# Kernel optimization log

Hardware: AMD Instinct MI355X
Metric: run time of the kernel (lower is better)

The kernel has to match this reference:

```python
import jax, jax.numpy as jnp
import numpy as np

D = 1024; DI = 2048; HS = 16; PS = DI // HS; NS = 64; KC = 4; CHUNK = 64
HA = 16; HKV = 4; PA = D // HA; MLP_MULT = 4; ROPE_BASE = 10000.0
B_SZ = 2; L_SEQ = 2048


def rms_norm(x):
    eps = jnp.asarray(jnp.finfo(x.dtype).eps, x.dtype)
    return x * jax.lax.rsqrt(jnp.mean(jnp.square(x), axis=-1, keepdims=True) + eps)


def silu(x):
    return x * jax.nn.sigmoid(x)


def apply_rope(x, cos, sin):
    half = x.shape[-1] // 2
    x1, x2 = x[..., :half], x[..., half:]
    return jnp.concatenate([x1 * cos + x2 * sin, -x1 * sin + x2 * cos], axis=-1)


def selective_scan(x, A, Bm, Cm, dt, chunk):
    # x: [B,L,H,P], Bm/Cm: [B,L,H,N], A/dt: [H]. L must be a multiple of chunk.
    Bb, L, H, P = x.shape
    N = Bm.shape[-1]
    decay = jnp.exp(A * dt)  # [H]
    nc = L // chunk
    xp = x.reshape(Bb, nc, chunk, H, P).transpose(0, 1, 3, 2, 4)   # [B,nc,H,cs,P]
    Bp = Bm.reshape(Bb, nc, chunk, H, N).transpose(0, 1, 3, 2, 4)  # [B,nc,H,cs,N]
    Cp = Cm.reshape(Bb, nc, chunk, H, N).transpose(0, 1, 3, 2, 4)
    x_dt = xp * dt[None, None, :, None, None]
    idx = jnp.arange(chunk)
    diff = idx[:, None] - idx[None, :]
    # intra-chunk causal decay matrix L_mat: [H,cs,cs]
    Lm = jnp.where(diff >= 0, decay[:, None, None] ** jnp.maximum(diff, 0), 0.0)
    CB = jnp.einsum('bchqn,bchkn->bchqk', Cp, Bp)
    y_diag = jnp.einsum('bchqk,bchkp->bchqp', CB * Lm[None, None], x_dt)
    # per-chunk states
    decay_rev = decay[:, None] ** (chunk - 1 - idx)[None, :]  # [H,cs]
    states = jnp.einsum('bchtn,bchtp->bchnp', Bp * decay_rev[None, None, :, :, None], x_dt)
    # inter-chunk propagation
    ci = jnp.arange(nc)
    shift = ci[:, None] - ci[None, :] - 1
    cdec = decay ** chunk
    M = jnp.where(shift >= 0, cdec[:, None, None] ** jnp.maximum(shift, 0), 0.0)  # [H,nc,nc]
    h_carry = jnp.einsum('hij,bjhnp->bihnp', M, states)
    decay_out = decay[:, None] ** (idx + 1)[None, :]  # [H,cs]
    y_off = jnp.einsum('bchtn,bchnp->bchtp', Cp, h_carry) * decay_out[None, None, :, :, None]
    y = (y_diag + y_off).transpose(0, 1, 3, 2, 4).reshape(Bb, L, H, P)
    return y


def mlp(n, fc_w, proj_w):
    h = jax.nn.relu(n @ fc_w)
    return jnp.square(h) @ proj_w


def setup_inputs() -> dict:
    key = jax.random.key(0)
    ks = jax.random.split(key, 24)
    w = lambda k, shp, s=0.02: jax.random.normal(k, shp, jnp.float32) * s
    dt_init = jax.random.uniform(ks[0], (HS,), jnp.float32, 0.001, 0.1)
    dt_bias = dt_init + jnp.log(-jnp.expm1(-dt_init))  # inverse softplus
    return {
        'x': jax.random.normal(ks[1], (B_SZ, L_SEQ, D), jnp.float32),
        'in_proj_w': w(ks[2], (D, 2 * DI)),
        'conv_w': w(ks[3], (DI, KC), 0.2),
        'conv_b': jnp.zeros((DI,), jnp.float32),
        'B_proj_w': w(ks[4], (D, HS * NS)),
        'C_proj_w': w(ks[5], (D, HS * NS)),
        'dt_bias': dt_bias,
        'A_log': jnp.log(jnp.arange(1, HS + 1, dtype=jnp.float32)),
        'D_param': jnp.ones((HS,), jnp.float32),
        'out_proj_w': w(ks[6], (DI, D)),
        'resid_mix_m': jnp.stack([jnp.ones(D), jnp.zeros(D)]).astype(jnp.float32),
        'mamba_scale': jnp.ones((D,), jnp.float32),
        'm_fc_w': w(ks[7], (D, MLP_MULT * D)),
        'm_proj_w': w(ks[8], (MLP_MULT * D, D)),
        'm_mlp_scale': jnp.ones((D,), jnp.float32),
        'resid_mix_a': jnp.stack([jnp.ones(D), jnp.zeros(D)]).astype(jnp.float32),
        'q_w': w(ks[9], (D, D)),
        'k_w': w(ks[10], (D, HKV * PA)),
        'v_w': w(ks[11], (D, HKV * PA)),
        'o_w': w(ks[12], (D, D)),
        'q_gain': jnp.full((HA,), 1.0, jnp.float32),
        'attn_scale': jnp.ones((D,), jnp.float32),
        'a_fc_w': w(ks[13], (D, MLP_MULT * D)),
        'a_proj_w': w(ks[14], (MLP_MULT * D, D)),
        'a_mlp_scale': jnp.ones((D,), jnp.float32),
    }


def reference(x, in_proj_w, conv_w, conv_b, B_proj_w, C_proj_w, dt_bias, A_log, D_param, out_proj_w, resid_mix_m, mamba_scale, m_fc_w, m_proj_w, m_mlp_scale, resid_mix_a, q_w, k_w, v_w, o_w, q_gain, attn_scale, a_fc_w, a_proj_w, a_mlp_scale):
    Bb, L, _ = x.shape
    x0 = x
    # ---- Mamba block ----
    xm = resid_mix_m[0][None, None] * x + resid_mix_m[1][None, None] * x0
    n = rms_norm(xm)
    vg = n @ in_proj_w
    value, gate = vg[..., :DI], vg[..., DI:]
    v_t = value.transpose(0, 2, 1)  # [B, DI, L]
    v_conv = jax.lax.conv_general_dilated(
        v_t, conv_w[:, None, :], (1,), [(KC - 1, 0)],
        feature_group_count=DI, dimension_numbers=('NCH', 'OIH', 'NCH')) + conv_b[None, :, None]
    value = silu(v_conv).transpose(0, 2, 1).reshape(Bb, L, HS, PS)
    Bm = (xm @ B_proj_w).reshape(Bb, L, HS, NS)  # B/C use pre-norm (mixed) input
    Cm = (xm @ C_proj_w).reshape(Bb, L, HS, NS)
    dt = jax.nn.softplus(dt_bias)
    A = -jnp.exp(A_log)
    y = selective_scan(value, A, Bm, Cm, dt, CHUNK)
    y = y + D_param[None, None, :, None] * value
    y = (y.reshape(Bb, L, DI) * silu(gate)) @ out_proj_w
    xm = xm + mamba_scale[None, None] * y
    xm = xm + m_mlp_scale[None, None] * mlp(rms_norm(xm), m_fc_w, m_proj_w)
    # ---- Attention block ----
    xa = resid_mix_a[0][None, None] * xm + resid_mix_a[1][None, None] * x0
    n = rms_norm(xa)
    q = (n @ q_w).reshape(Bb, L, HA, PA).transpose(0, 2, 1, 3)
    k = (n @ k_w).reshape(Bb, L, HKV, PA).transpose(0, 2, 1, 3)
    v = (n @ v_w).reshape(Bb, L, HKV, PA).transpose(0, 2, 1, 3)
    q = rms_norm(q); k = rms_norm(k)
    inv_freq = 1.0 / (ROPE_BASE ** (jnp.arange(0, PA, 2, dtype=jnp.float32) / PA))
    f = jnp.outer(jnp.arange(L, dtype=jnp.float32), inv_freq)
    cos, sin = jnp.cos(f)[None, None], jnp.sin(f)[None, None]
    q = apply_rope(q, cos, sin) * q_gain[None, :, None, None]
    k = apply_rope(k, cos, sin)
    G = HA // HKV
    k = jnp.repeat(k, G, axis=1); v = jnp.repeat(v, G, axis=1)
    s = jnp.einsum('bhqd,bhkd->bhqk', q, k) / np.float32(np.sqrt(PA))
    mask = jnp.tril(jnp.ones((L, L), bool))
    s = jnp.where(mask[None, None], s, jnp.asarray(-jnp.inf, s.dtype))
    att = jax.nn.softmax(s, axis=-1)
    y = jnp.einsum('bhqk,bhkd->bhqd', att, v).transpose(0, 2, 1, 3).reshape(Bb, L, D)
    xa = xa + attn_scale[None, None] * (y @ o_w)
    xa = xa + a_mlp_scale[None, None] * mlp(rms_norm(xa), a_fc_w, a_proj_w)
    return xa
```

## Files before the change

### kernel.cpp

```cpp
#include <hip/hip_runtime.h>
#include <hip/hip_bf16.h>
#include <math.h>

#define D_ 1024
#define DI_ 2048
#define HS_ 16
#define PS_ 128
#define NS_ 64
#define HA_ 16
#define HKV_ 4
#define PA_ 64
#define B_ 2
#define L_ 2048
#define NT_ 4096
#define NC_ 32
#define RMS_EPS_ 1.1920929e-7f

typedef __attribute__((ext_vector_type(8))) short short8;
typedef __attribute__((ext_vector_type(4))) float f32x4;

#define GLOAD_LDS16(gp, lp)                                                        \
  __builtin_amdgcn_global_load_lds(                                               \
      (const __attribute__((address_space(1))) unsigned int*)(gp),                \
      (__attribute__((address_space(3))) unsigned int*)(lp), 16, 0, 0)

__global__ __launch_bounds__(256) void transpose_cvt(
    const float* __restrict__ W, __hip_bfloat16* __restrict__ Wt, int K, int N, int ldw) {
  __shared__ float t[32][33];
  int n0 = blockIdx.x * 32, k0 = blockIdx.y * 32;
  int tx = threadIdx.x & 31, ty = threadIdx.x >> 5;
#pragma unroll
  for (int i = 0; i < 4; i++)
    t[ty + i * 8][tx] = W[(size_t)(k0 + ty + i * 8) * ldw + n0 + tx];
  __syncthreads();
#pragma unroll
  for (int i = 0; i < 4; i++)
    Wt[(size_t)(n0 + ty + i * 8) * K + k0 + tx] = __float2bfloat16(t[tx][ty + i * 8]);
}

template<int MODE>
__global__ __launch_bounds__(512) void gemm256_k32(
    const unsigned short* __restrict__ A, const unsigned short* __restrict__ Wt,
    __hip_bfloat16* __restrict__ Cb, int N, int K) {
  __shared__ unsigned short As[3][256 * 32];
  __shared__ unsigned short Bs[3][256 * 32];
  int lid = blockIdx.x;
  int x = lid & 7, r = lid >> 3;
  int bm = ((x >> 2) * 8 + (r & 7)) * 256;
  int bn = ((x & 3) * 4 + (r >> 3)) * 256;
  int tid = threadIdx.x;
  int w = tid >> 6, l = tid & 63;
  int wr = w >> 2, wc = w & 3;
  int l15 = l & 15, lg = l >> 4;
  int rr = tid >> 2, ss = tid & 3;

  f32x4 acc[8][4];
#pragma unroll
  for (int i = 0; i < 8; i++)
#pragma unroll
    for (int j = 0; j < 4; j++) acc[i][j] = (f32x4){0.f, 0.f, 0.f, 0.f};

  auto STAGE = [&](int kt, int nb) {
    int k0 = kt * 32;
#pragma unroll
    for (int p = 0; p < 2; p++) {
      int row = p * 128 + rr;
      int kq = ss ^ ((row >> 1) & 3);
      GLOAD_LDS16(A + (size_t)(bm + row) * K + k0 + kq * 8, &As[nb][row * 32 + ss * 8]);
    }
#pragma unroll
    for (int p = 0; p < 2; p++) {
      int row = p * 128 + rr;
      int kq = ss ^ ((row >> 1) & 3);
      GLOAD_LDS16(Wt + (size_t)(bn + row) * K + k0 + kq * 8, &Bs[nb][row * 32 + ss * 8]);
    }
  };

  int KT = K >> 5;
  STAGE(0, 0);
  STAGE(1, 1);
  int buf = 0;
  for (int t = 0; t < KT; ++t) {
    asm volatile("s_waitcnt vmcnt(4)" ::: "memory");
    __builtin_amdgcn_s_barrier();
    __builtin_amdgcn_sched_barrier(0);
    if (t + 2 < KT) STAGE(t + 2, (t + 2) % 3);
    short8 bf[4];
#pragma unroll
    for (int j = 0; j < 4; j++) {
      int row = wc * 64 + j * 16 + l15;
      bf[j] = *(const short8*)&Bs[buf][row * 32 + ((lg ^ ((row >> 1) & 3)) << 3)];
    }
#pragma unroll
    for (int i = 0; i < 8; i++) {
      int row = wr * 128 + i * 16 + l15;
      short8 af = *(const short8*)&As[buf][row * 32 + ((lg ^ ((row >> 1) & 3)) << 3)];
#pragma unroll
      for (int j = 0; j < 4; j++)
        acc[i][j] = __builtin_amdgcn_mfma_f32_16x16x32_bf16(af, bf[j], acc[i][j], 0, 0, 0);
    }
    buf = (buf + 1) % 3;
  }
#pragma unroll
  for (int i = 0; i < 8; i++)
#pragma unroll
    for (int j = 0; j < 4; j++) {
      int gr = bm + wr * 128 + i * 16 + lg * 4;
      int gc = bn + wc * 64 + j * 16 + l15;
#pragma unroll
      for (int reg = 0; reg < 4; reg++) {
        float v = acc[i][j][reg];
        if (MODE == 1) { v = fmaxf(v, 0.f); v = v * v; }
        Cb[(size_t)(gr + reg) * N + gc] = __float2bfloat16(v);
      }
    }
}

template<int BN>
__global__ __launch_bounds__(256) void gemm_bf16_t(
    const unsigned short* __restrict__ A, const unsigned short* __restrict__ Wt,
    float* __restrict__ Cf, __hip_bfloat16* __restrict__ Cb,
    const float* __restrict__ baseb, const float* __restrict__ scale,
    int N, int K, int gn, int mode) {
  constexpr int nWc = BN / 64;
  constexpr int nWr = 4 / nWc;
  constexpr int MF  = 8 / nWr;
  __shared__ unsigned short As[2][128 * 64];
  __shared__ unsigned short Bs[2][BN * 64];
  int lid = blockIdx.x;
  int x = lid & 7, r = lid >> 3;
  int RN = gn >> 2;
  int bm = ((x >> 2) * 16 + (r & 15)) * 128;
  int bn = ((x & 3) * RN + (r >> 4)) * BN;
  int tid = threadIdx.x;
  int w = tid >> 6, l = tid & 63;
  int wr = w / nWc, wc = w % nWc;
  int l15 = l & 15, lg = l >> 4;
  f32x4 acc[MF][4];
#pragma unroll
  for (int i = 0; i < MF; i++)
#pragma unroll
    for (int j = 0; j < 4; j++) acc[i][j] = (f32x4){0.f, 0.f, 0.f, 0.f};
  int r_ = tid >> 3;
  int s_ = tid & 7;

  auto STAGE = [&](int k0, int nb) {
#pragma unroll
    for (int i = 0; i < 4; i++) {
      int rr = i * 32 + r_;
      int kq = s_ ^ (rr & 7);
      GLOAD_LDS16(A + (size_t)(bm + rr) * K + k0 + kq * 8, &As[nb][rr * 64 + s_ * 8]);
    }
#pragma unroll
    for (int i = 0; i < BN / 32; i++) {
      int rr = i * 32 + r_;
      int kq = s_ ^ (rr & 7);
      GLOAD_LDS16(Wt + (size_t)(bn + rr) * K + k0 + kq * 8, &Bs[nb][rr * 64 + s_ * 8]);
    }
  };

  STAGE(0, 0);
  __syncthreads();
  int cur = 0;
  for (int k0 = 0; k0 < K; k0 += 64) {
    if (k0 + 64 < K) STAGE(k0 + 64, cur ^ 1);
#pragma unroll
    for (int h = 0; h < 2; h++) {
      short8 af[MF], bfr[4];
#pragma unroll
      for (int i = 0; i < MF; i++) {
        int row = wr * (16 * MF) + i * 16 + l15;
        int c = h * 4 + lg;
        af[i] = *(const short8*)&As[cur][row * 64 + ((c ^ (row & 7)) << 3)];
      }
#pragma unroll
      for (int j = 0; j < 4; j++) {
        int row = wc * 64 + j * 16 + l15;
        int c = h * 4 + lg;
        bfr[j] = *(const short8*)&Bs[cur][row * 64 + ((c ^ (row & 7)) << 3)];
      }
#pragma unroll
      for (int i = 0; i < MF; i++)
#pragma unroll
        for (int j = 0; j < 4; j++)
          acc[i][j] = __builtin_amdgcn_mfma_f32_16x16x32_bf16(af[i], bfr[j], acc[i][j], 0, 0, 0);
    }
    __syncthreads();
    cur ^= 1;
  }
  int rb = lg * 4, cb2 = l15;
#pragma unroll
  for (int i = 0; i < MF; i++)
#pragma unroll
    for (int j = 0; j < 4; j++) {
      int gr = bm + wr * (16 * MF) + i * 16 + rb;
      int gc = bn + wc * 64 + j * 16 + cb2;
#pragma unroll
      for (int reg = 0; reg < 4; reg++) {
        float v = acc[i][j][reg];
        size_t idx = (size_t)(gr + reg) * N + gc;
        if (mode == 0) {
          Cf[idx] = v;
        } else if (mode == 1) {
          v = fmaxf(v, 0.f);
          Cb[idx] = __float2bfloat16(v * v);
        } else if (mode == 2) {
          Cb[idx] = __float2bfloat16(v);
        } else {
          Cf[idx] = baseb[idx] + scale[gc] * v;
        }
      }
    }
}

__global__ __launch_bounds__(256) void mix_rms_kernel(
    const float* __restrict__ a, const float* __restrict__ b2,
    const float* __restrict__ mix, float* __restrict__ xout,
    __hip_bfloat16* __restrict__ nbf, __hip_bfloat16* __restrict__ rawbf) {
  int row = blockIdx.x;
  size_t base = (size_t)row * D_;
  float v[4]; float ss = 0.f;
#pragma unroll
  for (int i = 0; i < 4; i++) {
    int d = threadIdx.x + i * 256;
    float val = mix[d] * a[base + d] + mix[D_ + d] * b2[base + d];
    v[i] = val; ss += val * val;
  }
  for (int o = 32; o > 0; o >>= 1) ss += __shfl_down(ss, o, 64);
  __shared__ float red[4];
  if ((threadIdx.x & 63) == 0) red[threadIdx.x >> 6] = ss;
  __syncthreads();
  float inv = rsqrtf((red[0] + red[1] + red[2] + red[3]) * (1.f / D_) + RMS_EPS_);
#pragma unroll
  for (int i = 0; i < 4; i++) {
    int d = threadIdx.x + i * 256;
    xout[base + d] = v[i];
    nbf[base + d] = __float2bfloat16(v[i] * inv);
    if (rawbf) rawbf[base + d] = __float2bfloat16(v[i]);
  }
}

__global__ __launch_bounds__(256) void rms_kernel(
    const float* __restrict__ a, __hip_bfloat16* __restrict__ nbf) {
  int row = blockIdx.x;
  size_t base = (size_t)row * D_;
  float v[4]; float ss = 0.f;
#pragma unroll
  for (int i = 0; i < 4; i++) {
    int d = threadIdx.x + i * 256;
    float val = a[base + d];
    v[i] = val; ss += val * val;
  }
  for (int o = 32; o > 0; o >>= 1) ss += __shfl_down(ss, o, 64);
  __shared__ float red[4];
  if ((threadIdx.x & 63) == 0) red[threadIdx.x >> 6] = ss;
  __syncthreads();
  float inv = rsqrtf((red[0] + red[1] + red[2] + red[3]) * (1.f / D_) + RMS_EPS_);
#pragma unroll
  for (int i = 0; i < 4; i++) {
    int d = threadIdx.x + i * 256;
    nbf[base + d] = __float2bfloat16(v[i] * inv);
  }
}

__global__ __launch_bounds__(256) void conv_silu_kernel(
    const __hip_bfloat16* __restrict__ vg, const float* __restrict__ cw,
    const float* __restrict__ cb, float* __restrict__ xv) {
  int idx = blockIdx.x * 256 + threadIdx.x;
  int c = idx & (DI_ - 1);
  int bl = idx >> 11;
  int l = bl & (L_ - 1);
  float acc = cb[c];
  float w0 = cw[c * 4 + 0], w1 = cw[c * 4 + 1], w2 = cw[c * 4 + 2], w3 = cw[c * 4 + 3];
  size_t rb = (size_t)bl * 4096 + c;
  if (l >= 3) acc += __bfloat162float(vg[rb - (size_t)3 * 4096]) * w0;
  if (l >= 2) acc += __bfloat162float(vg[rb - (size_t)2 * 4096]) * w1;
  if (l >= 1) acc += __bfloat162float(vg[rb - (size_t)1 * 4096]) * w2;
  acc += __bfloat162float(vg[rb]) * w3;
  xv[idx] = acc / (1.f + __expf(-acc));
}

__global__ __launch_bounds__(256) void scanA1_kernel(
    const float* __restrict__ xv, const __hip_bfloat16* __restrict__ BCm,
    const float* __restrict__ dt_bias, const float* __restrict__ A_log,
    float* __restrict__ st) {
  __shared__ __align__(16) float sm[4096 + 8192];
  float* Bs = sm;
  float* Xs = sm + 4096;
  int blk = blockIdx.x;
  int c = blk & 31, h = (blk >> 5) & 15, b = blk >> 9;
  float dt = log1pf(__expf(dt_bias[h]));
  float adt = -__expf(A_log[h]) * dt;
  int tid = threadIdx.x;
  int l0 = c * 64;
  size_t rB = ((size_t)(b * L_ + l0)) * 2048 + h * NS_;
#pragma unroll
  for (int i = 0; i < 16; i++) {
    int e = tid + i * 256;
    int t = e >> 6, n = e & 63;
    Bs[t * 64 + n] = __bfloat162float(BCm[rB + (size_t)t * 2048 + n]);
  }
  size_t rX = ((size_t)(b * L_ + l0)) * DI_ + h * PS_;
#pragma unroll
  for (int i = 0; i < 32; i++) {
    int e = tid + i * 256;
    int t = e >> 7, p = e & 127;
    Xs[t * 128 + p] = xv[rX + (size_t)t * DI_ + p];
  }
  __syncthreads();
  int pg = tid & 31;
  int ng = (tid >> 5) << 3;
  float acc[8][4];
#pragma unroll
  for (int nn = 0; nn < 8; nn++)
#pragma unroll
    for (int i = 0; i < 4; i++) acc[nn][i] = 0.f;
  for (int t = 0; t < 64; t++) {
    float dr = __expf(adt * (float)(63 - t));
    float4 x4 = *(const float4*)&Xs[t * 128 + pg * 4];
    float xd0 = x4.x * dr, xd1 = x4.y * dr, xd2 = x4.z * dr, xd3 = x4.w * dr;
#pragma unroll
    for (int nn = 0; nn < 8; nn++) {
      float bv = Bs[t * 64 + ng + nn];
      acc[nn][0] += bv * xd0; acc[nn][1] += bv * xd1;
      acc[nn][2] += bv * xd2; acc[nn][3] += bv * xd3;
    }
  }
  size_t sb = ((size_t)((b * HS_ + h) * NC_ + c)) * (NS_ * PS_);
#pragma unroll
  for (int nn = 0; nn < 8; nn++) {
    *(float4*)&st[sb + (size_t)(ng + nn) * PS_ + pg * 4] =
        make_float4(acc[nn][0] * dt, acc[nn][1] * dt, acc[nn][2] * dt, acc[nn][3] * dt);
  }
}

__global__ __launch_bounds__(256) void scanA2_kernel(
    const float* __restrict__ xv, const __hip_bfloat16* __restrict__ BCm,
    const float* __restrict__ dt_bias,
    const float* __restrict__ A_log, const float* __restrict__ D_param,
    float* __restrict__ y) {
  __shared__ __align__(16) float sm[4160 + 8192];
  float* Cb = sm;
  float* Bs = sm + 4160;
  float* Xs = sm + 4160;
  int blk = blockIdx.x;
  int c = blk & 31, h = (blk >> 5) & 15, b = blk >> 9;
  float dt = log1pf(__expf(dt_bias[h]));
  float adt = -__expf(A_log[h]) * dt;
  float Dp = D_param[h];
  int tid = threadIdx.x;
  int l0 = c * 64;
  size_t rB = ((size_t)(b * L_ + l0)) * 2048 + h * NS_;
#pragma unroll
  for (int i = 0; i < 16; i++) {
    int e = tid + i * 256;
    int t = e >> 6, n = e & 63;
    Bs[t * 64 + n] = __bfloat162float(BCm[rB + (size_t)t * 2048 + n]);
    Cb[t * 65 + n] = __bfloat162float(BCm[rB + 1024 + (size_t)t * 2048 + n]);
  }
  __syncthreads();
  int q = tid >> 2;
  int kb = (tid & 3) << 4;
  float cbl[16];
#pragma unroll
  for (int kk = 0; kk < 16; kk++) {
    int k = kb + kk;
    float a = 0.f;
    if (k <= q) {
      for (int n = 0; n < 64; n++) a += Cb[q * 65 + n] * Bs[k * 64 + n];
      a *= __expf(adt * (float)(q - k));
    }
    cbl[kk] = a;
  }
  __syncthreads();
#pragma unroll
  for (int kk = 0; kk < 16; kk++) Cb[q * 65 + kb + kk] = cbl[kk];
  size_t rX = ((size_t)(b * L_ + l0)) * DI_ + h * PS_;
#pragma unroll
  for (int i = 0; i < 32; i++) {
    int e = tid + i * 256;
    int t = e >> 7, p = e & 127;
    Xs[t * 128 + p] = xv[rX + (size_t)t * DI_ + p];
  }
  __syncthreads();
  int pg = tid & 31;
  int qg = (tid >> 5) << 3;
  float acc[8][4];
#pragma unroll
  for (int qq = 0; qq < 8; qq++)
#pragma unroll
    for (int i = 0; i < 4; i++) acc[qq][i] = 0.f;
  for (int k = 0; k < 64; k++) {
    float4 x4 = *(const float4*)&Xs[k * 128 + pg * 4];
#pragma unroll
    for (int qq = 0; qq < 8; qq++) {
      float s = Cb[(qg + qq) * 65 + k];
      acc[qq][0] += s * x4.x; acc[qq][1] += s * x4.y;
      acc[qq][2] += s * x4.z; acc[qq][3] += s * x4.w;
    }
  }
#pragma unroll
  for (int qq = 0; qq < 8; qq++) {
    int qr = qg + qq;
    float4 xq = *(const float4*)&Xs[qr * 128 + pg * 4];
    size_t yo = ((size_t)(b * L_ + l0 + qr)) * DI_ + h * PS_ + pg * 4;
    *(float4*)&y[yo] = make_float4(acc[qq][0] * dt + Dp * xq.x,
                                   acc[qq][1] * dt + Dp * xq.y,
                                   acc[qq][2] * dt + Dp * xq.z,
                                   acc[qq][3] * dt + Dp * xq.w);
  }
}

__global__ __launch_bounds__(256) void scanB1_kernel(
    float* __restrict__ st, const float* __restrict__ dt_bias,
    const float* __restrict__ A_log) {
  int slice = blockIdx.x & 3;
  int h = (blockIdx.x >> 2) & 15, b = blockIdx.x >> 6;
  float dt = log1pf(__expf(dt_bias[h]));
  float adt = -__expf(A_log[h]) * dt;
  float cdec = __expf(adt * 64.f);
  size_t base = ((size_t)(b * HS_ + h)) * NC_ * (NS_ * PS_) + slice * 2048 + threadIdx.x;
  float hreg[8];
#pragma unroll
  for (int j = 0; j < 8; j++) hreg[j] = 0.f;
  for (int c = 0; c < NC_; c++) {
    size_t o = base + (size_t)c * (NS_ * PS_);
#pragma unroll
    for (int j = 0; j < 8; j++) {
      float tmp = st[o + (size_t)j * 256];
      st[o + (size_t)j * 256] = hreg[j];
      hreg[j] = cdec * hreg[j] + tmp;
    }
  }
}

__global__ __launch_bounds__(256) void scanB2_kernel(
    const __hip_bfloat16* __restrict__ BCm, const float* __restrict__ st,
    const __hip_bfloat16* __restrict__ vg, const float* __restrict__ dt_bias,
    const float* __restrict__ A_log, const float* __restrict__ y,
    __hip_bfloat16* __restrict__ yout) {
  __shared__ float Cs[64 * 64];
  __shared__ __align__(16) float Hs[64 * 128];
  int blk = blockIdx.x;
  int c = blk & 31, h = (blk >> 5) & 15, b = blk >> 9;
  float dt = log1pf(__expf(dt_bias[h]));
  float adt = -__expf(A_log[h]) * dt;
  int tid = threadIdx.x;
  int l0 = c * 64;
  size_t rC = ((size_t)(b * L_ + l0)) * 2048 + 1024 + h * NS_;
#pragma unroll
  for (int i = 0; i < 16; i++) {
    int e = tid + i * 256;
    int t = e >> 6, n = e & 63;
    Cs[t * 64 + n] = __bfloat162float(BCm[rC + (size_t)t * 2048 + n]);
  }
  size_t sb = ((size_t)((b * HS_ + h) * NC_ + c)) * (NS_ * PS_);
#pragma unroll
  for (int i = 0; i < 32; i++) {
    int e = tid + i * 256;
    Hs[e] = st[sb + e];
  }
  __syncthreads();
  int pg = tid & 31;
  int tg = (tid >> 5) << 3;
  float acc[8][4];
#pragma unroll
  for (int tt = 0; tt < 8; tt++)
#pragma unroll
    for (int i = 0; i < 4; i++) acc[tt][i] = 0.f;
  for (int n = 0; n < 64; n++) {
    float4 h4 = *(const float4*)&Hs[n * 128 + pg * 4];
#pragma unroll
    for (int tt = 0; tt < 8; tt++) {
      float cv = Cs[(tg + tt) * 64 + n];
      acc[tt][0] += cv * h4.x; acc[tt][1] += cv * h4.y;
      acc[tt][2] += cv * h4.z; acc[tt][3] += cv * h4.w;
    }
  }
#pragma unroll
  for (int tt = 0; tt < 8; tt++) {
    int t = tg + tt;
    float dout = __expf(adt * (float)(t + 1));
    size_t row = (size_t)(b * L_ + l0 + t);
#pragma unroll
    for (int i = 0; i < 4; i++) {
      int p = pg * 4 + i;
      float g = __bfloat162float(vg[row * 4096 + 2048 + h * PS_ + p]);
      float yv = y[row * DI_ + h * PS_ + p] + acc[tt][i] * dout;
      yout[row * DI_ + h * PS_ + p] = __float2bfloat16(yv * (g / (1.f + __expf(-g))));
    }
  }
}

__global__ void rope_fill_kernel(float* __restrict__ cosb, float* __restrict__ sinb) {
  int idx = blockIdx.x * 256 + threadIdx.x;
  int i = idx & 31, l = idx >> 5;
  float inv = __expf(-(2.0f * (float)i / (float)PA_) * logf(10000.0f));
  float ang = (float)l * inv;
  cosb[idx] = cosf(ang);
  sinb[idx] = sinf(ang);
}

__global__ __launch_bounds__(256) void qknorm_rope_bf16_kernel(
    const float* __restrict__ src, int srcstride, int srcofs,
    __hip_bfloat16* __restrict__ dst, int nh,
    const float* __restrict__ cosb, const float* __restrict__ sinb,
    const float* __restrict__ gain) {
  int row = blockIdx.x * 4 + (threadIdx.x >> 6);
  int lane = threadIdx.x & 63;
  int h = row % nh;
  int tok = row / nh;
  int l = tok & (L_ - 1);
  float v = src[(size_t)tok * srcstride + srcofs + h * 64 + lane];
  float ss = v * v;
  for (int o = 32; o > 0; o >>= 1) ss += __shfl_xor(ss, o, 64);
  v *= rsqrtf(ss * (1.f / PA_) + RMS_EPS_);
  float partner = __shfl_xor(v, 32, 64);
  int i = lane & 31;
  float cth = cosb[l * 32 + i], sth = sinb[l * 32 + i];
  float out = (lane < 32) ? (v * cth + partner * sth) : (v * cth - partner * sth);
  if (gain) out *= gain[h];
  dst[(size_t)tok * (nh * 64) + h * 64 + lane] = __float2bfloat16(out);
}

__global__ __launch_bounds__(256) void attn_mfma_kernel(
    const unsigned short* __restrict__ qb, const unsigned short* __restrict__ kb,
    const unsigned short* __restrict__ vt, const float* __restrict__ qgain,
    __hip_bfloat16* __restrict__ ao) {
  __shared__ unsigned short Ks[64][72];
  __shared__ unsigned short Vs[64][72];
  __shared__ unsigned short Psm[4][16][72];
  int blk = blockIdx.x;
  int qi = blk & 15;
  int h  = (blk >> 4) & 15;
  int b  = blk >> 8;
  int hk = h >> 2;
  int tid = threadIdx.x;
  int w = tid >> 6, l = tid & 63;
  int l15 = l & 15, lg = l >> 4;
  int r0 = tid >> 3, s0 = tid & 7;
  float mstat = 8.0f * fabsf(qgain[h]);
  const unsigned short* kbase = kb + (size_t)b * L_ * (HKV_ * PA_) + hk * PA_ + s0 * 8;
  const unsigned short* vbase = vt + ((size_t)(b * HKV_ + hk) * PA_) * L_ + s0 * 8;

  for (int pass = 0; pass < 2; pass++) {
    int qt = pass ? (31 - qi) : qi;
    int q0 = qt * 64;
    int qw = q0 + w * 16;
    short8 qf[2];
    {
      size_t qrow = ((size_t)(b * L_ + qw + l15)) * (HA_ * PA_) + h * PA_;
      qf[0] = *(const short8*)&qb[qrow + lg * 8];
      qf[1] = *(const short8*)&qb[qrow + 32 + lg * 8];
    }
    f32x4 o_acc[4];
#pragma unroll
    for (int db = 0; db < 4; db++) o_acc[db] = (f32x4){0.f, 0.f, 0.f, 0.f};
    f32x4 lsum = (f32x4){0.f, 0.f, 0.f, 0.f};
    int nkt = qt + 1;
    short8 kr0 = *(const short8*)&kbase[(size_t)r0 * (HKV_ * PA_)];
    short8 kr1 = *(const short8*)&kbase[(size_t)(r0 + 32) * (HKV_ * PA_)];
    short8 vr0 = *(const short8*)&vbase[(size_t)r0 * L_];
    short8 vr1 = *(const short8*)&vbase[(size_t)(r0 + 32) * L_];
    for (int kt = 0; kt < nkt; kt++) {
      int k0 = kt * 64;
      __syncthreads();
      *(short8*)&Ks[r0][s0 * 8] = kr0;
      *(short8*)&Ks[r0 + 32][s0 * 8] = kr1;
      *(short8*)&Vs[r0][s0 * 8] = vr0;
      *(short8*)&Vs[r0 + 32][s0 * 8] = vr1;
      if (kt + 1 < nkt) {
        int k1 = k0 + 64;
        kr0 = *(const short8*)&kbase[(size_t)(k1 + r0) * (HKV_ * PA_)];
        kr1 = *(const short8*)&kbase[(size_t)(k1 + r0 + 32) * (HKV_ * PA_)];
        vr0 = *(const short8*)&vbase[(size_t)r0 * L_ + k1];
        vr1 = *(const short8*)&vbase[(size_t)(r0 + 32) * L_ + k1];
      }
      __syncthreads();
      f32x4 s_acc[4];
#pragma unroll
      for (int kb2 = 0; kb2 < 4; kb2++) {
        short8 b0 = *(const short8*)&Ks[kb2 * 16 + l15][lg * 8];
        short8 b1 = *(const short8*)&Ks[kb2 * 16 + l15][32 + lg * 8];
        f32x4 s = (f32x4){0.f, 0.f, 0.f, 0.f};
        s = __builtin_amdgcn_mfma_f32_16x16x32_bf16(qf[0], b0, s, 0, 0, 0);
        s = __builtin_amdgcn_mfma_f32_16x16x32_bf16(qf[1], b1, s, 0, 0, 0);
        s_acc[kb2] = s;
      }
      bool diag = (kt == qt);
#pragma unroll
      for (int kb2 = 0; kb2 < 4; kb2++) {
        int key = k0 + kb2 * 16 + l15;
#pragma unroll
        for (int reg = 0; reg < 4; reg++) {
          float p = __expf(s_acc[kb2][reg] * 0.125f - mstat);
          if (diag && key > qw + lg * 4 + reg) p = 0.f;
          lsum[reg] += p;
          __hip_bfloat16 hv = __float2bfloat16(p);
          Psm[w][lg * 4 + reg][kb2 * 16 + l15] = *(unsigned short*)&hv;
        }
      }
      asm volatile("s_waitcnt lgkmcnt(0)" ::: "memory");
#pragma unroll
      for (int ks = 0; ks < 2; ks++) {
        short8 pa = *(const short8*)&Psm[w][l15][ks * 32 + lg * 8];
#pragma unroll
        for (int db = 0; db < 4; db++) {
          short8 vb8 = *(const short8*)&Vs[db * 16 + l15][ks * 32 + lg * 8];
          o_acc[db] = __builtin_amdgcn_mfma_f32_16x16x32_bf16(pa, vb8, o_acc[db], 0, 0, 0);
        }
      }
    }
#pragma unroll
    for (int of = 1; of < 16; of <<= 1) {
      lsum[0] += __shfl_xor(lsum[0], of, 64);
      lsum[1] += __shfl_xor(lsum[1], of, 64);
      lsum[2] += __shfl_xor(lsum[2], of, 64);
      lsum[3] += __shfl_xor(lsum[3], of, 64);
    }
#pragma unroll
    for (int reg = 0; reg < 4; reg++) {
      float invl = 1.0f / lsum[reg];
      size_t row = (size_t)(b * L_ + qw + lg * 4 + reg);
#pragma unroll
      for (int db = 0; db < 4; db++)
        ao[row * D_ + h * PA_ + db * 16 + l15] = __float2bfloat16(o_acc[db][reg] * invl);
    }
  }
}

extern "C" void kernel_launch(void* const* d_in, const int* in_sizes, int n_in,
                              void* d_out, int out_size, void* d_ws, size_t ws_size,
                              hipStream_t stream) {
  (void)in_sizes; (void)n_in; (void)out_size; (void)ws_size;
  const float* x           = (const float*)d_in[0];
  const float* in_proj_w   = (const float*)d_in[1];
  const float* conv_w      = (const float*)d_in[2];
  const float* conv_b      = (const float*)d_in[3];
  const float* B_proj_w    = (const float*)d_in[4];
  const float* C_proj_w    = (const float*)d_in[5];
  const float* dt_bias     = (const float*)d_in[6];
  const float* A_log       = (const float*)d_in[7];
  const float* D_param     = (const float*)d_in[8];
  const float* out_proj_w  = (const float*)d_in[9];
  const float* resid_mix_m = (const float*)d_in[10];
  const float* mamba_scale = (const float*)d_in[11];
  const float* m_fc_w      = (const float*)d_in[12];
  const float* m_proj_w    = (const float*)d_in[13];
  const float* m_mlp_scale = (const float*)d_in[14];
  const float* resid_mix_a = (const float*)d_in[15];
  const float* q_w         = (const float*)d_in[16];
  const float* k_w         = (const float*)d_in[17];
  const float* v_w         = (const float*)d_in[18];
  const float* o_w         = (const float*)d_in[19];
  const float* q_gain      = (const float*)d_in[20];
  const float* attn_scale  = (const float*)d_in[21];
  const float* a_fc_w      = (const float*)d_in[22];
  const float* a_proj_w    = (const float*)d_in[23];
  const float* a_mlp_scale = (const float*)d_in[24];
  float* ws  = (float*)d_ws;
  float* out = (float*)d_out;

  float* xm    = ws;
  float* vgR   = ws + 4194304;
  float* xvR   = ws + 12582912;
  float* stR   = ws + 20971520;
  float* nbR   = ws + 29360128;
  float* xmbR  = ws + 31457280;
  float* BCR   = ws + 33554432;
  float* WtR   = ws + 37748736;
  float* cosb  = ws + 51642368;
  float* sinb  = cosb + 65536;

  __hip_bfloat16* vg  = (__hip_bfloat16*)vgR;
  float*          qkvf = vgR;
  float*          xv  = xvR;
  float*          st  = stR;
  __hip_bfloat16* hb  = (__hip_bfloat16*)stR;
  __hip_bfloat16* nbb = (__hip_bfloat16*)nbR;
  __hip_bfloat16* xmb = (__hip_bfloat16*)xmbR;
  __hip_bfloat16* ybb = (__hip_bfloat16*)nbR;
  __hip_bfloat16* BCm = (__hip_bfloat16*)BCR;
  __hip_bfloat16* qbb = (__hip_bfloat16*)xvR;
  __hip_bfloat16* kbb = (__hip_bfloat16*)(xvR + 2097152);
  __hip_bfloat16* vtb = (__hip_bfloat16*)(xvR + 2621440);
  __hip_bfloat16* aob = (__hip_bfloat16*)(xvR + 3145728);

  __hip_bfloat16* Wt = (__hip_bfloat16*)WtR;
  size_t o_in  = 0;
  size_t o_B   = o_in  + (size_t)4096 * 1024;
  size_t o_out = o_B   + (size_t)2048 * 1024;
  size_t o_mfc = o_out + (size_t)1024 * 2048;
  size_t o_mpj = o_mfc + (size_t)4096 * 1024;
  size_t o_qkv = o_mpj + (size_t)1024 * 4096;
  size_t o_o   = o_qkv + (size_t)1536 * 1024;
  size_t o_afc = o_o   + (size_t)1024 * 1024;
  size_t o_apj = o_afc + (size_t)4096 * 1024;

#define TCVT(Wp, off, K, N) \
  transpose_cvt<<<dim3((N) / 32, (K) / 32), 256, 0, stream>>>((Wp), Wt + (off), (K), (N), (N))
  TCVT(in_proj_w,  o_in,  1024, 4096);
  TCVT(B_proj_w,   o_B,   1024, 1024);
  TCVT(C_proj_w,   o_B + (size_t)1024 * 1024, 1024, 1024);
  TCVT(out_proj_w, o_out, 2048, 1024);
  TCVT(m_fc_w,     o_mfc, 1024, 4096);
  TCVT(m_proj_w,   o_mpj, 4096, 1024);
  TCVT(q_w,        o_qkv, 1024, 1024);
  TCVT(k_w,        o_qkv + (size_t)1024 * 1024, 1024, 256);
  TCVT(v_w,        o_qkv + (size_t)1280 * 1024, 1024, 256);
  TCVT(o_w,        o_o,   1024, 1024);
  TCVT(a_fc_w,     o_afc, 1024, 4096);
  TCVT(a_proj_w,   o_apj, 4096, 1024);
#undef TCVT

#define GEMM(BN, Abuf, Woff, Cfp, Cbp, basep, scalep, N, K, mode) \
  gemm_bf16_t<BN><<<32 * ((N) / (BN)), 256, 0, stream>>>( \
      (const unsigned short*)(Abuf), (const unsigned short*)(Wt + (Woff)), \
      (Cfp), (Cbp), (basep), (scalep), (N), (K), (N) / (BN), (mode))
#define GEMM256(MODE, Abuf, Woff, Cbp) \
  gemm256_k32<MODE><<<256, 512, 0, stream>>>( \
      (const unsigned short*)(Abuf), (const unsigned short*)(Wt + (Woff)), \
      (Cbp), 4096, 1024)

  mix_rms_kernel<<<NT_, 256, 0, stream>>>(x, x, resid_mix_m, xm, nbb, xmb);
  GEMM256(2, nbb, o_in, vg);
  GEMM(128, xmb, o_B, (float*)0, BCm, (const float*)0, (const float*)0, 2048, 1024, 2);
  conv_silu_kernel<<<NT_ * DI_ / 256, 256, 0, stream>>>(vg, conv_w, conv_b, xv);
  scanA1_kernel<<<B_ * HS_ * NC_, 256, 0, stream>>>(xv, BCm, dt_bias, A_log, st);
  scanA2_kernel<<<B_ * HS_ * NC_, 256, 0, stream>>>(xv, BCm, dt_bias, A_log, D_param, xv);
  scanB1_kernel<<<B_ * HS_ * 4, 256, 0, stream>>>(st, dt_bias, A_log);
  scanB2_kernel<<<B_ * HS_ * NC_, 256, 0, stream>>>(BCm, st, vg, dt_bias, A_log, xv, ybb);
  GEMM(64, ybb, o_out, xm, (__hip_bfloat16*)0, xm, mamba_scale, 1024, 2048, 3);
  rms_kernel<<<NT_, 256, 0, stream>>>(xm, nbb);
  GEMM256(1, nbb, o_mfc, hb);
  GEMM(64, hb, o_mpj, xm, (__hip_bfloat16*)0, xm, m_mlp_scale, 1024, 4096, 3);
  mix_rms_kernel<<<NT_, 256, 0, stream>>>(xm, x, resid_mix_a, xm, nbb, (__hip_bfloat16*)0);
  GEMM(64, nbb, o_qkv, qkvf, (__hip_bfloat16*)0, (const float*)0, (const float*)0, 1536, 1024, 0);
  rope_fill_kernel<<<L_ * 32 / 256, 256, 0, stream>>>(cosb, sinb);
  qknorm_rope_bf16_kernel<<<NT_ * HA_ / 4, 256, 0, stream>>>(qkvf, 1536, 0, qbb, HA_, cosb, sinb, q_gain);
  qknorm_rope_bf16_kernel<<<NT_ * HKV_ / 4, 256, 0, stream>>>(qkvf, 1536, 1024, kbb, HKV_, cosb, sinb, (const float*)0);
  transpose_cvt<<<dim3(256 / 32, 2048 / 32), 256, 0, stream>>>(qkvf + 1280, vtb, 2048, 256, 1536);
  transpose_cvt<<<dim3(256 / 32, 2048 / 32), 256, 0, stream>>>(qkvf + (size_t)L_ * 1536 + 1280, vtb + (size_t)256 * L_, 2048, 256, 1536);
  attn_mfma_kernel<<<B_ * HA_ * 16, 256, 0, stream>>>(
      (const unsigned short*)qbb, (const unsigned short*)kbb, (const unsigned short*)vtb,
      q_gain, aob);
  GEMM(64, aob, o_o, xm, (__hip_bfloat16*)0, xm, attn_scale, 1024, 1024, 3);
  rms_kernel<<<NT_, 256, 0, stream>>>(xm, nbb);
  GEMM256(1, nbb, o_afc, hb);
  GEMM(64, hb, o_apj, out, (__hip_bfloat16*)0, xm, a_mlp_scale, 1024, 4096, 3);
#undef GEMM
#undef GEMM256
}
```

Measured before the change: 680.6 us.

## Convert templated GEMM to triple-buffered BK=32 pipeline with vmcnt waits

The generic bf16 GEMM drops its double-buffered BK=64 loop with two __syncthreads per step. It now uses a three-stage BK=32 ring with two tiles prefetched ahead, partial s_waitcnt vmcnt waits and a single barrier per iteration, matching the other GEMM kernel. The last iteration waits for all loads (vmcnt 0), and that final-wait fix is also applied to the existing kernel. This is meant to hide global-to-LDS load latency better and cut barrier overhead, at the cost of more, smaller k-iterations and hand-tuned vmcnt counts that must match the number of loads issued per stage.

```diff
diff --git a/kernel.cpp b/kernel.cpp
--- a/kernel.cpp
+++ b/kernel.cpp
@@ -81,7 +81,11 @@
   STAGE(1, 1);
   int buf = 0;
   for (int t = 0; t < KT; ++t) {
-    asm volatile("s_waitcnt vmcnt(4)" ::: "memory");
+    if (t + 1 < KT) {
+      asm volatile("s_waitcnt vmcnt(4)" ::: "memory");
+    } else {
+      asm volatile("s_waitcnt vmcnt(0)" ::: "memory");
+    }
     __builtin_amdgcn_s_barrier();
     __builtin_amdgcn_sched_barrier(0);
     if (t + 2 < KT) STAGE(t + 2, (t + 2) % 3);
@@ -99,7 +103,7 @@
       for (int j = 0; j < 4; j++)
         acc[i][j] = __builtin_amdgcn_mfma_f32_16x16x32_bf16(af, bf[j], acc[i][j], 0, 0, 0);
     }
-    buf = (buf + 1) % 3;
+    buf = (buf == 2) ? 0 : buf + 1;
   }
 #pragma unroll
   for (int i = 0; i < 8; i++)
@@ -125,8 +129,8 @@
   constexpr int nWc = BN / 64;
   constexpr int nWr = 4 / nWc;
   constexpr int MF  = 8 / nWr;
-  __shared__ unsigned short As[2][128 * 64];
-  __shared__ unsigned short Bs[2][BN * 64];
+  __shared__ unsigned short As[3][128 * 32];
+  __shared__ unsigned short Bs[3][BN * 32];
   int lid = blockIdx.x;
   int x = lid & 7, r = lid >> 3;
   int RN = gn >> 2;
@@ -136,57 +140,60 @@
   int w = tid >> 6, l = tid & 63;
   int wr = w / nWc, wc = w % nWc;
   int l15 = l & 15, lg = l >> 4;
+  int rr = tid >> 2, ss = tid & 3;
   f32x4 acc[MF][4];
 #pragma unroll
   for (int i = 0; i < MF; i++)
 #pragma unroll
     for (int j = 0; j < 4; j++) acc[i][j] = (f32x4){0.f, 0.f, 0.f, 0.f};
-  int r_ = tid >> 3;
-  int s_ = tid & 7;
-
-  auto STAGE = [&](int k0, int nb) {
-#pragma unroll
-    for (int i = 0; i < 4; i++) {
-      int rr = i * 32 + r_;
-      int kq = s_ ^ (rr & 7);
-      GLOAD_LDS16(A + (size_t)(bm + rr) * K + k0 + kq * 8, &As[nb][rr * 64 + s_ * 8]);
-    }
-#pragma unroll
-    for (int i = 0; i < BN / 32; i++) {
-      int rr = i * 32 + r_;
-      int kq = s_ ^ (rr & 7);
-      GLOAD_LDS16(Wt + (size_t)(bn + rr) * K + k0 + kq * 8, &Bs[nb][rr * 64 + s_ * 8]);
+
+  auto STAGE = [&](int kt, int nb) {
+    int k0 = kt * 32;
+#pragma unroll
+    for (int p = 0; p < 2; p++) {
+      int row = p * 64 + rr;
+      int kq = ss ^ ((row >> 1) & 3);
+      GLOAD_LDS16(A + (size_t)(bm + row) * K + k0 + kq * 8, &As[nb][row * 32 + ss * 8]);
+    }
+#pragma unroll
+    for (int p = 0; p < BN / 64; p++) {
+      int row = p * 64 + rr;
+      int kq = ss ^ ((row >> 1) & 3);
+      GLOAD_LDS16(Wt + (size_t)(bn + row) * K + k0 + kq * 8, &Bs[nb][row * 32 + ss * 8]);
     }
   };
 
+  int KT = K >> 5;
   STAGE(0, 0);
-  __syncthreads();
-  int cur = 0;
-  for (int k0 = 0; k0 < K; k0 += 64) {
-    if (k0 + 64 < K) STAGE(k0 + 64, cur ^ 1);
-#pragma unroll
-    for (int h = 0; h < 2; h++) {
-      short8 af[MF], bfr[4];
-#pragma unroll
-      for (int i = 0; i < MF; i++) {
-        int row = wr * (16 * MF) + i * 16 + l15;
-        int c = h * 4 + lg;
-        af[i] = *(const short8*)&As[cur][row * 64 + ((c ^ (row & 7)) << 3)];
-      }
-#pragma unroll
-      for (int j = 0; j < 4; j++) {
-        int row = wc * 64 + j * 16 + l15;
-        int c = h * 4 + lg;
-        bfr[j] = *(const short8*)&Bs[cur][row * 64 + ((c ^ (row & 7)) << 3)];
-      }
-#pragma unroll
-      for (int i = 0; i < MF; i++)
-#pragma unroll
-        for (int j = 0; j < 4; j++)
-          acc[i][j] = __builtin_amdgcn_mfma_f32_16x16x32_bf16(af[i], bfr[j], acc[i][j], 0, 0, 0);
-    }
-    __syncthreads();
-    cur ^= 1;
+  STAGE(1, 1);
+  int buf = 0;
+  for (int t = 0; t < KT; ++t) {
+    if (t + 1 < KT) {
+      if constexpr (BN == 64) asm volatile("s_waitcnt vmcnt(3)" ::: "memory");
+      else                    asm volatile("s_waitcnt vmcnt(4)" ::: "memory");
+    } else {
+      asm volatile("s_waitcnt vmcnt(0)" ::: "memory");
+    }
+    __builtin_amdgcn_s_barrier();
+    __builtin_amdgcn_sched_barrier(0);
+    if (t + 2 < KT) STAGE(t + 2, (t + 2) % 3);
+    short8 af[MF], bfr[4];
+#pragma unroll
+    for (int j = 0; j < 4; j++) {
+      int row = wc * 64 + j * 16 + l15;
+      bfr[j] = *(const short8*)&Bs[buf][row * 32 + ((lg ^ ((row >> 1) & 3)) << 3)];
+    }
+#pragma unroll
+    for (int i = 0; i < MF; i++) {
+      int row = wr * (16 * MF) + i * 16 + l15;
+      af[i] = *(const short8*)&As[buf][row * 32 + ((lg ^ ((row >> 1) & 3)) << 3)];
+    }
+#pragma unroll
+    for (int i = 0; i < MF; i++)
+#pragma unroll
+      for (int j = 0; j < 4; j++)
+        acc[i][j] = __builtin_amdgcn_mfma_f32_16x16x32_bf16(af[i], bfr[j], acc[i][j], 0, 0, 0);
+    buf = (buf == 2) ? 0 : buf + 1;
   }
   int rb = lg * 4, cb2 = l15;
 #pragma unroll
```

Result: slower. 717.3 us (+5.4%).

## Split-K residual GEMMs with atomic accumulation and tune B/C projection tile

Applied to the files above, without the earlier changes.

Adds a split-K mode to the generic bf16 GEMM that halves the K range per block and accumulates scaled results into the residual buffer with atomic adds. This doubles the grid for the N=1024 output projections to improve CU occupancy. The final residual is seeded by copying xm into out inside the RMS kernel. The B/C projection switches from a 128-wide to a 64-wide tile, and the 256-tile GEMM's last iteration now waits for all loads. Atomic float adds make summation order nondeterministic and add read-modify-write traffic.

```diff
diff --git a/kernel.cpp b/kernel.cpp
--- a/kernel.cpp
+++ b/kernel.cpp
@@ -81,7 +81,11 @@
   STAGE(1, 1);
   int buf = 0;
   for (int t = 0; t < KT; ++t) {
-    asm volatile("s_waitcnt vmcnt(4)" ::: "memory");
+    if (t + 1 < KT) {
+      asm volatile("s_waitcnt vmcnt(4)" ::: "memory");
+    } else {
+      asm volatile("s_waitcnt vmcnt(0)" ::: "memory");
+    }
     __builtin_amdgcn_s_barrier();
     __builtin_amdgcn_sched_barrier(0);
     if (t + 2 < KT) STAGE(t + 2, (t + 2) % 3);
@@ -99,7 +103,7 @@
       for (int j = 0; j < 4; j++)
         acc[i][j] = __builtin_amdgcn_mfma_f32_16x16x32_bf16(af, bf[j], acc[i][j], 0, 0, 0);
     }
-    buf = (buf + 1) % 3;
+    buf = (buf == 2) ? 0 : buf + 1;
   }
 #pragma unroll
   for (int i = 0; i < 8; i++)
@@ -121,17 +125,22 @@
     const unsigned short* __restrict__ A, const unsigned short* __restrict__ Wt,
     float* __restrict__ Cf, __hip_bfloat16* __restrict__ Cb,
     const float* __restrict__ baseb, const float* __restrict__ scale,
-    int N, int K, int gn, int mode) {
+    int N, int K, int gn, int mode, int ksplit) {
   constexpr int nWc = BN / 64;
   constexpr int nWr = 4 / nWc;
   constexpr int MF  = 8 / nWr;
   __shared__ unsigned short As[2][128 * 64];
   __shared__ unsigned short Bs[2][BN * 64];
   int lid = blockIdx.x;
-  int x = lid & 7, r = lid >> 3;
+  int x = lid & 7;
+  int ks = 0, r;
+  if (ksplit) { ks = (lid >> 3) & 1; r = lid >> 4; }
+  else        { r = lid >> 3; }
   int RN = gn >> 2;
   int bm = ((x >> 2) * 16 + (r & 15)) * 128;
   int bn = ((x & 3) * RN + (r >> 4)) * BN;
+  int KH = ksplit ? (K >> 1) : K;
+  int kbeg = ks * KH;
   int tid = threadIdx.x;
   int w = tid >> 6, l = tid & 63;
   int wr = w / nWc, wc = w % nWc;
@@ -159,11 +168,11 @@
     }
   };
 
-  STAGE(0, 0);
+  STAGE(kbeg, 0);
   __syncthreads();
   int cur = 0;
-  for (int k0 = 0; k0 < K; k0 += 64) {
-    if (k0 + 64 < K) STAGE(k0 + 64, cur ^ 1);
+  for (int k0 = kbeg; k0 < kbeg + KH; k0 += 64) {
+    if (k0 + 64 < kbeg + KH) STAGE(k0 + 64, cur ^ 1);
 #pragma unroll
     for (int h = 0; h < 2; h++) {
       short8 af[MF], bfr[4];
@@ -206,8 +215,10 @@
           Cb[idx] = __float2bfloat16(v * v);
         } else if (mode == 2) {
           Cb[idx] = __float2bfloat16(v);
+        } else if (mode == 3) {
+          Cf[idx] = baseb[idx] + scale[gc] * v;
         } else {
-          Cf[idx] = baseb[idx] + scale[gc] * v;
+          unsafeAtomicAdd(&Cf[idx], scale[gc] * v);
         }
       }
     }
@@ -241,7 +252,8 @@
 }
 
 __global__ __launch_bounds__(256) void rms_kernel(
-    const float* __restrict__ a, __hip_bfloat16* __restrict__ nbf) {
+    const float* __restrict__ a, __hip_bfloat16* __restrict__ nbf,
+    float* __restrict__ copyout) {
   int row = blockIdx.x;
   size_t base = (size_t)row * D_;
   float v[4]; float ss = 0.f;
@@ -260,6 +272,7 @@
   for (int i = 0; i < 4; i++) {
     int d = threadIdx.x + i * 256;
     nbf[base + d] = __float2bfloat16(v[i] * inv);
+    if (copyout) copyout[base + d] = v[i];
   }
 }
 
@@ -713,10 +726,10 @@
   TCVT(a_proj_w,   o_apj, 4096, 1024);
 #undef TCVT
 
-#define GEMM(BN, Abuf, Woff, Cfp, Cbp, basep, scalep, N, K, mode) \
-  gemm_bf16_t<BN><<<32 * ((N) / (BN)), 256, 0, stream>>>( \
+#define GEMM(BN, Abuf, Woff, Cfp, Cbp, basep, scalep, N, K, mode, ksp) \
+  gemm_bf16_t<BN><<<(1 + (ksp)) * 32 * ((N) / (BN)), 256, 0, stream>>>( \
       (const unsigned short*)(Abuf), (const unsigned short*)(Wt + (Woff)), \
-      (Cfp), (Cbp), (basep), (scalep), (N), (K), (N) / (BN), (mode))
+      (Cfp), (Cbp), (basep), (scalep), (N), (K), (N) / (BN), (mode), (ksp))
 #define GEMM256(MODE, Abuf, Woff, Cbp) \
   gemm256_k32<MODE><<<256, 512, 0, stream>>>( \
       (const unsigned short*)(Abuf), (const unsigned short*)(Wt + (Woff)), \
@@ -724,18 +737,18 @@
 
   mix_rms_kernel<<<NT_, 256, 0, stream>>>(x, x, resid_mix_m, xm, nbb, xmb);
   GEMM256(2, nbb, o_in, vg);
-  GEMM(128, xmb, o_B, (float*)0, BCm, (const float*)0, (const float*)0, 2048, 1024, 2);
+  GEMM(64, xmb, o_B, (float*)0, BCm, (const float*)0, (const float*)0, 2048, 1024, 2, 0);
   conv_silu_kernel<<<NT_ * DI_ / 256, 256, 0, stream>>>(vg, conv_w, conv_b, xv);
   scanA1_kernel<<<B_ * HS_ * NC_, 256, 0, stream>>>(xv, BCm, dt_bias, A_log, st);
   scanA2_kernel<<<B_ * HS_ * NC_, 256, 0, stream>>>(xv, BCm, dt_bias, A_log, D_param, xv);
   scanB1_kernel<<<B_ * HS_ * 4, 256, 0, stream>>>(st, dt_bias, A_log);
   scanB2_kernel<<<B_ * HS_ * NC_, 256, 0, stream>>>(BCm, st, vg, dt_bias, A_log, xv, ybb);
-  GEMM(64, ybb, o_out, xm, (__hip_bfloat16*)0, xm, mamba_scale, 1024, 2048, 3);
-  rms_kernel<<<NT_, 256, 0, stream>>>(xm, nbb);
+  GEMM(64, ybb, o_out, xm, (__hip_bfloat16*)0, (const float*)0, mamba_scale, 1024, 2048, 4, 1);
+  rms_kernel<<<NT_, 256, 0, stream>>>(xm, nbb, (float*)0);
   GEMM256(1, nbb, o_mfc, hb);
-  GEMM(64, hb, o_mpj, xm, (__hip_bfloat16*)0, xm, m_mlp_scale, 1024, 4096, 3);
+  GEMM(64, hb, o_mpj, xm, (__hip_bfloat16*)0, (const float*)0, m_mlp_scale, 1024, 4096, 4, 1);
   mix_rms_kernel<<<NT_, 256, 0, stream>>>(xm, x, resid_mix_a, xm, nbb, (__hip_bfloat16*)0);
-  GEMM(64, nbb, o_qkv, qkvf, (__hip_bfloat16*)0, (const float*)0, (const float*)0, 1536, 1024, 0);
+  GEMM(64, nbb, o_qkv, qkvf, (__hip_bfloat16*)0, (const float*)0, (const float*)0, 1536, 1024, 0, 0);
   rope_fill_kernel<<<L_ * 32 / 256, 256, 0, stream>>>(cosb, sinb);
   qknorm_rope_bf16_kernel<<<NT_ * HA_ / 4, 256, 0, stream>>>(qkvf, 1536, 0, qbb, HA_, cosb, sinb, q_gain);
   qknorm_rope_bf16_kernel<<<NT_ * HKV_ / 4, 256, 0, stream>>>(qkvf, 1536, 1024, kbb, HKV_, cosb, sinb, (const float*)0);
@@ -744,10 +757,10 @@
   attn_mfma_kernel<<<B_ * HA_ * 16, 256, 0, stream>>>(
       (const unsigned short*)qbb, (const unsigned short*)kbb, (const unsigned short*)vtb,
       q_gain, aob);
-  GEMM(64, aob, o_o, xm, (__hip_bfloat16*)0, xm, attn_scale, 1024, 1024, 3);
-  rms_kernel<<<NT_, 256, 0, stream>>>(xm, nbb);
+  GEMM(64, aob, o_o, xm, (__hip_bfloat16*)0, (const float*)0, attn_scale, 1024, 1024, 4, 1);
+  rms_kernel<<<NT_, 256, 0, stream>>>(xm, nbb, out);
   GEMM256(1, nbb, o_afc, hb);
-  GEMM(64, hb, o_apj, out, (__hip_bfloat16*)0, xm, a_mlp_scale, 1024, 4096, 3);
+  GEMM(64, hb, o_apj, out, (__hip_bfloat16*)0, (const float*)0, a_mlp_scale, 1024, 4096, 4, 1);
 #undef GEMM
 #undef GEMM256
 }
```

Result: slower. 791.3 us (+16.3%).
